# Kernel tuning notes

Hardware: AMD Instinct MI355X
Metric: run time of the kernel (lower is better)

The kernel has to match this reference:

```python
import jax, jax.numpy as jnp
import numpy as np

S = 100   # n_pred_samples
B = 64    # batch
DIMS = [784, 512, 512, 10]


def setup_inputs() -> dict:
    key = jax.random.key(0)
    ks = jax.random.split(key, 16)
    d = {}
    d["inputs"] = jax.random.normal(ks[0], (B, DIMS[0]), dtype=jnp.float32)
    d["task_id"] = 0
    # variational params: means ~ 0.1*N(0,1), logvars constant -6 (as in module init)
    d["wm0"] = jax.random.normal(ks[1], (DIMS[0], DIMS[1])) * 0.1
    d["wv0"] = jnp.full((DIMS[0], DIMS[1]), -6.0, jnp.float32)
    d["bm0"] = jnp.full((DIMS[1],), 0.1, jnp.float32)
    d["bv0"] = jnp.full((DIMS[1],), -6.0, jnp.float32)
    d["wm1"] = jax.random.normal(ks[2], (DIMS[1], DIMS[2])) * 0.1
    d["wv1"] = jnp.full((DIMS[1], DIMS[2]), -6.0, jnp.float32)
    d["bm1"] = jnp.full((DIMS[2],), 0.1, jnp.float32)
    d["bv1"] = jnp.full((DIMS[2],), -6.0, jnp.float32)
    d["wml"] = jax.random.normal(ks[3], (DIMS[2], DIMS[3])) * 0.1
    d["wvl"] = jnp.full((DIMS[2], DIMS[3]), -6.0, jnp.float32)
    d["bml"] = jnp.full((DIMS[3],), 0.1, jnp.float32)
    d["bvl"] = jnp.full((DIMS[3],), -6.0, jnp.float32)
    # reparameterization noise (passed explicitly for determinism)
    d["we0"] = jax.random.normal(ks[4], (S, DIMS[0], DIMS[1]), dtype=jnp.float32)
    d["be0"] = jax.random.normal(ks[5], (S, 1, DIMS[1]), dtype=jnp.float32)
    d["we1"] = jax.random.normal(ks[6], (S, DIMS[1], DIMS[2]), dtype=jnp.float32)
    d["be1"] = jax.random.normal(ks[7], (S, 1, DIMS[2]), dtype=jnp.float32)
    d["wel"] = jax.random.normal(ks[8], (S, DIMS[2], DIMS[3]), dtype=jnp.float32)
    d["bel"] = jax.random.normal(ks[9], (S, 1, DIMS[3]), dtype=jnp.float32)
    return d


def _sample(eps, logvar, mean):
    # reparameterization: eps * exp(0.5*logvar) + mean
    return eps * jnp.exp(0.5 * logvar) + mean


def reference(inputs, task_id, wm0, wv0, bm0, bv0, wm1, wv1, bm1, bv1,
              wml, wvl, bml, bvl, we0, be0, we1, be1, wel, bel):
    # activations: [S, B, D]
    act = jnp.broadcast_to(inputs[None], (S,) + inputs.shape)
    # hidden layer 0
    W0 = _sample(we0, wv0, wm0)          # [S, D0, D1]
    b0 = _sample(be0, bv0, bm0)          # [S, 1, D1]
    act = jax.nn.relu(jnp.einsum('sbi,sio->sbo', act, W0) + b0)
    # hidden layer 1
    W1 = _sample(we1, wv1, wm1)
    b1 = _sample(be1, bv1, bm1)
    act = jax.nn.relu(jnp.einsum('sbi,sio->sbo', act, W1) + b1)
    # last (task-specific) layer: original does broadcast-mul + sum over dim 2,
    # which is exactly a batched matmul — expressed here as an einsum
    Wl = _sample(wel, wvl, wml)          # [S, D2, O]
    bl = _sample(bel, bvl, bml)          # [S, 1, O]
    logits = jnp.einsum('sbh,sho->sbo', act, Wl) + bl   # [S, B, O]
    return logits
```

## Files before the change

### kernel.cpp

```cpp
#include <hip/hip_runtime.h>
#include <hip/hip_bf16.h>


typedef __bf16 bf16x8 __attribute__((ext_vector_type(8)));
typedef float f32x4 __attribute__((ext_vector_type(4)));

#define NSAMP 100
#define BATCH 64
#define D0 784
#define D1 512
#define D2 512
#define DOUT 10
#define K0PAD 800

#define BM 64
#define BN 64
#define BK 32
#define LDK 36

__device__ __forceinline__ unsigned short f2bf(float f) {
    __bf16 b = (__bf16)f;
    return __builtin_bit_cast(unsigned short, b);
}

union FragU { uint2 d[2]; bf16x8 v; };

#define XB_N   (BATCH * K0PAD)
#define SG0_N  (D0 * D1)
#define SG1_N  (D1 * D2)
#define SGL_N  (D2 * DOUT)
#define B0_N   (NSAMP * D1)
#define B1_N   (NSAMP * D2)
#define BL_N   (NSAMP * DOUT)
#define PREP_TOTAL (XB_N + SG0_N + SG1_N + SGL_N + B0_N + B1_N + BL_N)

__global__ __launch_bounds__(256) void prep(
    const float* __restrict__ inputs,
    const float* __restrict__ wv0, const float* __restrict__ wv1,
    const float* __restrict__ wvl,
    const float* __restrict__ be0, const float* __restrict__ bv0, const float* __restrict__ bm0,
    const float* __restrict__ be1, const float* __restrict__ bv1, const float* __restrict__ bm1,
    const float* __restrict__ bel, const float* __restrict__ bvl, const float* __restrict__ bml,
    unsigned short* __restrict__ Xb, float* __restrict__ sigma0,
    float* __restrict__ sigma1, float* __restrict__ sigmal,
    float* __restrict__ bias0, float* __restrict__ bias1, float* __restrict__ biasl)
{
    int i = blockIdx.x * 256 + threadIdx.x;
    if (i < XB_N) {
        int m = i / K0PAD, k = i % K0PAD;
        float v = (k < D0) ? inputs[m * D0 + k] : 0.f;
        Xb[i] = f2bf(v);
        return;
    }
    i -= XB_N;
    if (i < SG0_N) { sigma0[i] = __expf(0.5f * wv0[i]); return; }
    i -= SG0_N;
    if (i < SG1_N) { sigma1[i] = __expf(0.5f * wv1[i]); return; }
    i -= SG1_N;
    if (i < SGL_N) { sigmal[i] = __expf(0.5f * wvl[i]); return; }
    i -= SGL_N;
    if (i < B0_N) { int n = i % D1; bias0[i] = fmaf(be0[i], __expf(0.5f * bv0[n]), bm0[n]); return; }
    i -= B0_N;
    if (i < B1_N) { int n = i % D2; bias1[i] = fmaf(be1[i], __expf(0.5f * bv1[n]), bm1[n]); return; }
    i -= B1_N;
    if (i < BL_N) { int o = i % DOUT; biasl[i] = fmaf(bel[i], __expf(0.5f * bvl[o]), bml[o]); return; }
}

__global__ __launch_bounds__(256) void gemm_layer(
    const unsigned short* __restrict__ A, int lda, long aStride,
    const float* __restrict__ eps, long eStride,
    const float* __restrict__ sigma, const float* __restrict__ mean,
    int N, int K, int Kvalid,
    const float* __restrict__ bias,
    void* __restrict__ outp, int outBf16)
{
    __shared__ unsigned short smA[BM * LDK];
    __shared__ unsigned short smB[BN * LDK];

    const int s  = blockIdx.y;
    const int n0 = blockIdx.x * BN;
    const int t  = threadIdx.x;

    const unsigned short* As = A + (long)s * aStride;
    const float* epsS = eps + (long)s * eStride;

    const int am = t >> 2;
    const int ac = (t & 3) * 8;
    const int bn  = t & 63;
    const int bk0 = (t >> 6) * 8;

    const int lane = t & 63;
    const int w    = t >> 6;
    const int mbase = (w & 1) * 32;
    const int nbase = (w >> 1) * 32;
    const int fr   = lane & 15;
    const int quad = lane >> 4;

    f32x4 acc[2][2] = {};
    const int KT = K / BK;

    uint4 pa;
    float pe[8], ps[8], pm[8];

    {
        pa = *reinterpret_cast<const uint4*>(As + (long)am * lda + ac);
#pragma unroll
        for (int j = 0; j < 8; ++j) {
            int k = bk0 + j;
            long off = (long)k * N + n0 + bn;
            bool v = k < Kvalid;
            pe[j] = v ? epsS[off] : 0.f;
            ps[j] = v ? sigma[off] : 0.f;
            pm[j] = v ? mean[off] : 0.f;
        }
    }

    for (int kt = 0; kt < KT; ++kt) {
        __syncthreads();
        {
            unsigned short* dst = &smA[am * LDK + ac];
            uint2 w0; w0.x = pa.x; w0.y = pa.y;
            uint2 w1; w1.x = pa.z; w1.y = pa.w;
            reinterpret_cast<uint2*>(dst)[0] = w0;
            *reinterpret_cast<uint2*>(dst + 4) = w1;
        }
        {
            unsigned int p01, p23, p45, p67;
            p01 = (unsigned int)f2bf(fmaf(pe[0], ps[0], pm[0])) |
                  ((unsigned int)f2bf(fmaf(pe[1], ps[1], pm[1])) << 16);
            p23 = (unsigned int)f2bf(fmaf(pe[2], ps[2], pm[2])) |
                  ((unsigned int)f2bf(fmaf(pe[3], ps[3], pm[3])) << 16);
            p45 = (unsigned int)f2bf(fmaf(pe[4], ps[4], pm[4])) |
                  ((unsigned int)f2bf(fmaf(pe[5], ps[5], pm[5])) << 16);
            p67 = (unsigned int)f2bf(fmaf(pe[6], ps[6], pm[6])) |
                  ((unsigned int)f2bf(fmaf(pe[7], ps[7], pm[7])) << 16);
            unsigned short* dst = &smB[bn * LDK + bk0];
            uint2 w0; w0.x = p01; w0.y = p23;
            uint2 w1; w1.x = p45; w1.y = p67;
            reinterpret_cast<uint2*>(dst)[0] = w0;
            *reinterpret_cast<uint2*>(dst + 4) = w1;
        }
        if (kt + 1 < KT) {
            const int kg = (kt + 1) * BK;
            pa = *reinterpret_cast<const uint4*>(As + (long)am * lda + kg + ac);
#pragma unroll
            for (int j = 0; j < 8; ++j) {
                int k = kg + bk0 + j;
                long off = (long)k * N + n0 + bn;
                bool v = k < Kvalid;
                pe[j] = v ? epsS[off] : 0.f;
                ps[j] = v ? sigma[off] : 0.f;
                pm[j] = v ? mean[off] : 0.f;
            }
        }
        __syncthreads();
        FragU af[2], bf[2];
#pragma unroll
        for (int mi = 0; mi < 2; ++mi) {
            const unsigned short* p = &smA[(mbase + mi * 16 + fr) * LDK + quad * 8];
            const uint2* q = reinterpret_cast<const uint2*>(p);
            af[mi].d[0] = q[0]; af[mi].d[1] = q[1];
        }
#pragma unroll
        for (int ni = 0; ni < 2; ++ni) {
            const unsigned short* p = &smB[(nbase + ni * 16 + fr) * LDK + quad * 8];
            const uint2* q = reinterpret_cast<const uint2*>(p);
            bf[ni].d[0] = q[0]; bf[ni].d[1] = q[1];
        }
#pragma unroll
        for (int mi = 0; mi < 2; ++mi)
#pragma unroll
            for (int ni = 0; ni < 2; ++ni)
                acc[mi][ni] = __builtin_amdgcn_mfma_f32_16x16x32_bf16(
                    af[mi].v, bf[ni].v, acc[mi][ni], 0, 0, 0);
    }

    const long outBase = (long)s * BATCH * N;
#pragma unroll
    for (int mi = 0; mi < 2; ++mi) {
#pragma unroll
        for (int ni = 0; ni < 2; ++ni) {
            const int col = n0 + nbase + ni * 16 + fr;
            const float bv = bias[(long)s * N + col];
#pragma unroll
            for (int r = 0; r < 4; ++r) {
                const int row = mbase + mi * 16 + quad * 4 + r;
                float v = acc[mi][ni][r] + bv;
                v = fmaxf(v, 0.f);
                const long idx = outBase + (long)row * N + col;
                if (outBf16) ((unsigned short*)outp)[idx] = f2bf(v);
                else         ((float*)outp)[idx] = v;
            }
        }
    }
}

__global__ __launch_bounds__(320) void last_layer(
    const float* __restrict__ act2,
    const float* __restrict__ wel,
    const float* __restrict__ sigmal,
    const float* __restrict__ wml,
    const float* __restrict__ biasl,
    float* __restrict__ out)
{
    __shared__ float smW[D2 * DOUT];
    const int s = blockIdx.x;
    const int t = threadIdx.x;
    const float* we = wel + (long)s * D2 * DOUT;
    for (int i = t; i < D2 * DOUT; i += 320)
        smW[i] = fmaf(we[i], sigmal[i], wml[i]);
    __syncthreads();

    const int m  = t / 5;
    const int op = t % 5;
    const float* a = act2 + ((long)s * BATCH + m) * D2;
    float acc0 = 0.f, acc1 = 0.f;
#pragma unroll 4
    for (int k = 0; k < D2; k += 4) {
        float4 av = *reinterpret_cast<const float4*>(a + k);
        acc0 = fmaf(av.x, smW[(k + 0) * DOUT + op], acc0);
        acc0 = fmaf(av.y, smW[(k + 1) * DOUT + op], acc0);
        acc0 = fmaf(av.z, smW[(k + 2) * DOUT + op], acc0);
        acc0 = fmaf(av.w, smW[(k + 3) * DOUT + op], acc0);
        acc1 = fmaf(av.x, smW[(k + 0) * DOUT + op + 5], acc1);
        acc1 = fmaf(av.y, smW[(k + 1) * DOUT + op + 5], acc1);
        acc1 = fmaf(av.z, smW[(k + 2) * DOUT + op + 5], acc1);
        acc1 = fmaf(av.w, smW[(k + 3) * DOUT + op + 5], acc1);
    }
    const long ob = ((long)s * BATCH + m) * DOUT;
    out[ob + op]     = acc0 + biasl[s * DOUT + op];
    out[ob + op + 5] = acc1 + biasl[s * DOUT + op + 5];
}

extern "C" void kernel_launch(void* const* d_in, const int* in_sizes, int n_in,
                              void* d_out, int out_size, void* d_ws, size_t ws_size,
                              hipStream_t stream)
{
    const float* inputs = (const float*)d_in[0];
    const float* wm0 = (const float*)d_in[2];
    const float* wv0 = (const float*)d_in[3];
    const float* bm0 = (const float*)d_in[4];
    const float* bv0 = (const float*)d_in[5];
    const float* wm1 = (const float*)d_in[6];
    const float* wv1 = (const float*)d_in[7];
    const float* bm1 = (const float*)d_in[8];
    const float* bv1 = (const float*)d_in[9];
    const float* wml = (const float*)d_in[10];
    const float* wvl = (const float*)d_in[11];
    const float* bml = (const float*)d_in[12];
    const float* bvl = (const float*)d_in[13];
    const float* we0 = (const float*)d_in[14];
    const float* be0 = (const float*)d_in[15];
    const float* we1 = (const float*)d_in[16];
    const float* be1 = (const float*)d_in[17];
    const float* wel = (const float*)d_in[18];
    const float* bel = (const float*)d_in[19];

    char* w = (char*)d_ws;
    unsigned short* Xb = (unsigned short*)w; w += (size_t)XB_N * 2;
    float* sigma0 = (float*)w; w += (size_t)SG0_N * 4;
    float* sigma1 = (float*)w; w += (size_t)SG1_N * 4;
    float* sigmal = (float*)w; w += (size_t)SGL_N * 4;
    float* bias0  = (float*)w; w += (size_t)B0_N * 4;
    float* bias1  = (float*)w; w += (size_t)B1_N * 4;
    float* biasl  = (float*)w; w += (size_t)BL_N * 4;
    unsigned short* act1 = (unsigned short*)w; w += (size_t)NSAMP * BATCH * D1 * 2;
    float* act2 = (float*)w; w += (size_t)NSAMP * BATCH * D2 * 4;

    prep<<<dim3((PREP_TOTAL + 255) / 256), 256, 0, stream>>>(
        inputs, wv0, wv1, wvl, be0, bv0, bm0, be1, bv1, bm1, bel, bvl, bml,
        Xb, sigma0, sigma1, sigmal, bias0, bias1, biasl);

    gemm_layer<<<dim3(D1 / BN, NSAMP), 256, 0, stream>>>(
        Xb, K0PAD, 0L, we0, (long)D0 * D1, sigma0, wm0,
        D1, K0PAD, D0, bias0, (void*)act1, 1);

    gemm_layer<<<dim3(D2 / BN, NSAMP), 256, 0, stream>>>(
        act1, D1, (long)BATCH * D1, we1, (long)D1 * D2, sigma1, wm1,
        D2, D1, D1, bias1, (void*)act2, 0);

    last_layer<<<dim3(NSAMP), 320, 0, stream>>>(
        act2, wel, sigmal, wml, biasl, (float*)d_out);
}
```

Measured before the change: 411.0 us.

## Pack sigma/mean as bf16 pairs and use per-wave register GEMM without LDS

Prep now packs the bf16 sigma and bf16 mean for layers 0 and 1 into one 32-bit word, so the GEMM reads one word per weight instead of two floats. The block-tiled LDS GEMM is replaced by a kernel where each wave owns a 16-column strip of one sample across all 64 rows. Fragments load straight from global memory into registers with double-buffered prefetch, and eps uses nontemporal loads, which removes LDS staging and __syncthreads. The cost is that A is reloaded by every wave, and sigma and mean drop to bf16 precision before the reparameterisation FMA.

```diff
diff --git a/kernel.cpp b/kernel.cpp
--- a/kernel.cpp
+++ b/kernel.cpp
@@ -13,36 +13,39 @@
 #define DOUT 10
 #define K0PAD 800
 
-#define BM 64
-#define BN 64
-#define BK 32
-#define LDK 36
-
 __device__ __forceinline__ unsigned short f2bf(float f) {
     __bf16 b = (__bf16)f;
     return __builtin_bit_cast(unsigned short, b);
 }
-
-union FragU { uint2 d[2]; bf16x8 v; };
+__device__ __forceinline__ float bf_hi(unsigned int u) {
+    return __builtin_bit_cast(float, u & 0xffff0000u);
+}
+__device__ __forceinline__ float bf_lo(unsigned int u) {
+    return __builtin_bit_cast(float, u << 16);
+}
+
+union FragU { uint2 d[2]; uint4 q; bf16x8 v; };
 
 #define XB_N   (BATCH * K0PAD)
-#define SG0_N  (D0 * D1)
-#define SG1_N  (D1 * D2)
+#define PS0_N  (D0 * D1)
+#define PS1_N  (D1 * D2)
 #define SGL_N  (D2 * DOUT)
 #define B0_N   (NSAMP * D1)
 #define B1_N   (NSAMP * D2)
 #define BL_N   (NSAMP * DOUT)
-#define PREP_TOTAL (XB_N + SG0_N + SG1_N + SGL_N + B0_N + B1_N + BL_N)
+#define PREP_TOTAL (XB_N + PS0_N + PS1_N + SGL_N + B0_N + B1_N + BL_N)
 
 __global__ __launch_bounds__(256) void prep(
     const float* __restrict__ inputs,
-    const float* __restrict__ wv0, const float* __restrict__ wv1,
+    const float* __restrict__ wv0, const float* __restrict__ wm0,
+    const float* __restrict__ wv1, const float* __restrict__ wm1,
     const float* __restrict__ wvl,
     const float* __restrict__ be0, const float* __restrict__ bv0, const float* __restrict__ bm0,
     const float* __restrict__ be1, const float* __restrict__ bv1, const float* __restrict__ bm1,
     const float* __restrict__ bel, const float* __restrict__ bvl, const float* __restrict__ bml,
-    unsigned short* __restrict__ Xb, float* __restrict__ sigma0,
-    float* __restrict__ sigma1, float* __restrict__ sigmal,
+    unsigned short* __restrict__ Xb,
+    unsigned int* __restrict__ psm0, unsigned int* __restrict__ psm1,
+    float* __restrict__ sigmal,
     float* __restrict__ bias0, float* __restrict__ bias1, float* __restrict__ biasl)
 {
     int i = blockIdx.x * 256 + threadIdx.x;
@@ -53,10 +56,20 @@
         return;
     }
     i -= XB_N;
-    if (i < SG0_N) { sigma0[i] = __expf(0.5f * wv0[i]); return; }
-    i -= SG0_N;
-    if (i < SG1_N) { sigma1[i] = __expf(0.5f * wv1[i]); return; }
-    i -= SG1_N;
+    if (i < PS0_N) {
+        unsigned int sg = f2bf(__expf(0.5f * wv0[i]));
+        unsigned int mn = f2bf(wm0[i]);
+        psm0[i] = (sg << 16) | mn;
+        return;
+    }
+    i -= PS0_N;
+    if (i < PS1_N) {
+        unsigned int sg = f2bf(__expf(0.5f * wv1[i]));
+        unsigned int mn = f2bf(wm1[i]);
+        psm1[i] = (sg << 16) | mn;
+        return;
+    }
+    i -= PS1_N;
     if (i < SGL_N) { sigmal[i] = __expf(0.5f * wvl[i]); return; }
     i -= SGL_N;
     if (i < B0_N) { int n = i % D1; bias0[i] = fmaf(be0[i], __expf(0.5f * bv0[n]), bm0[n]); return; }
@@ -66,131 +79,89 @@
     if (i < BL_N) { int o = i % DOUT; biasl[i] = fmaf(bel[i], __expf(0.5f * bvl[o]), bml[o]); return; }
 }
 
-__global__ __launch_bounds__(256) void gemm_layer(
+__global__ __launch_bounds__(256) void gemm_wave(
     const unsigned short* __restrict__ A, int lda, long aStride,
     const float* __restrict__ eps, long eStride,
-    const float* __restrict__ sigma, const float* __restrict__ mean,
-    int N, int K, int Kvalid,
+    const unsigned int* __restrict__ psm,
+    int KT, int Kvalid,
     const float* __restrict__ bias,
     void* __restrict__ outp, int outBf16)
 {
-    __shared__ unsigned short smA[BM * LDK];
-    __shared__ unsigned short smB[BN * LDK];
-
-    const int s  = blockIdx.y;
-    const int n0 = blockIdx.x * BN;
-    const int t  = threadIdx.x;
-
-    const unsigned short* As = A + (long)s * aStride;
-    const float* epsS = eps + (long)s * eStride;
-
-    const int am = t >> 2;
-    const int ac = (t & 3) * 8;
-    const int bn  = t & 63;
-    const int bk0 = (t >> 6) * 8;
-
-    const int lane = t & 63;
-    const int w    = t >> 6;
-    const int mbase = (w & 1) * 32;
-    const int nbase = (w >> 1) * 32;
+    const int N = 512;
+    const int wid  = blockIdx.x * 4 + (threadIdx.x >> 6);
+    const int s    = wid >> 5;
+    const int n0   = (wid & 31) << 4;
+    const int lane = threadIdx.x & 63;
     const int fr   = lane & 15;
     const int quad = lane >> 4;
 
-    f32x4 acc[2][2] = {};
-    const int KT = K / BK;
-
-    uint4 pa;
-    float pe[8], ps[8], pm[8];
-
-    {
-        pa = *reinterpret_cast<const uint4*>(As + (long)am * lda + ac);
+    const unsigned short* aP = A + (long)s * aStride + (long)fr * lda + quad * 8;
+    const long bbase = (long)(quad * 8) * N + n0 + fr;
+    const float* eP        = eps + (long)s * eStride + bbase;
+    const unsigned int* pP = psm + bbase;
+
+    f32x4 acc[4] = {};
+    const bool tail = (Kvalid < KT * 32);
+
+    uint4 pa0[4], pa1[4];
+    float pe0[8], pe1[8];
+    unsigned int pp0[8], pp1[8];
+
+    auto loadAll = [&](int kt, uint4* pa, float* pe, unsigned int* pp) {
+        const int kb = kt * 32;
+        const bool guard = tail && (kt == KT - 1);
+#pragma unroll
+        for (int sub = 0; sub < 4; ++sub)
+            pa[sub] = *reinterpret_cast<const uint4*>(aP + (long)sub * 16 * lda + kb);
 #pragma unroll
         for (int j = 0; j < 8; ++j) {
-            int k = bk0 + j;
-            long off = (long)k * N + n0 + bn;
-            bool v = k < Kvalid;
-            pe[j] = v ? epsS[off] : 0.f;
-            ps[j] = v ? sigma[off] : 0.f;
-            pm[j] = v ? mean[off] : 0.f;
-        }
-    }
-
-    for (int kt = 0; kt < KT; ++kt) {
-        __syncthreads();
-        {
-            unsigned short* dst = &smA[am * LDK + ac];
-            uint2 w0; w0.x = pa.x; w0.y = pa.y;
-            uint2 w1; w1.x = pa.z; w1.y = pa.w;
-            reinterpret_cast<uint2*>(dst)[0] = w0;
-            *reinterpret_cast<uint2*>(dst + 4) = w1;
-        }
-        {
-            unsigned int p01, p23, p45, p67;
-            p01 = (unsigned int)f2bf(fmaf(pe[0], ps[0], pm[0])) |
-                  ((unsigned int)f2bf(fmaf(pe[1], ps[1], pm[1])) << 16);
-            p23 = (unsigned int)f2bf(fmaf(pe[2], ps[2], pm[2])) |
-                  ((unsigned int)f2bf(fmaf(pe[3], ps[3], pm[3])) << 16);
-            p45 = (unsigned int)f2bf(fmaf(pe[4], ps[4], pm[4])) |
-                  ((unsigned int)f2bf(fmaf(pe[5], ps[5], pm[5])) << 16);
-            p67 = (unsigned int)f2bf(fmaf(pe[6], ps[6], pm[6])) |
-                  ((unsigned int)f2bf(fmaf(pe[7], ps[7], pm[7])) << 16);
-            unsigned short* dst = &smB[bn * LDK + bk0];
-            uint2 w0; w0.x = p01; w0.y = p23;
-            uint2 w1; w1.x = p45; w1.y = p67;
-            reinterpret_cast<uint2*>(dst)[0] = w0;
-            *reinterpret_cast<uint2*>(dst + 4) = w1;
-        }
-        if (kt + 1 < KT) {
-            const int kg = (kt + 1) * BK;
-            pa = *reinterpret_cast<const uint4*>(As + (long)am * lda + kg + ac);
-#pragma unroll
-            for (int j = 0; j < 8; ++j) {
-                int k = kg + bk0 + j;
-                long off = (long)k * N + n0 + bn;
-                bool v = k < Kvalid;
-                pe[j] = v ? epsS[off] : 0.f;
-                ps[j] = v ? sigma[off] : 0.f;
-                pm[j] = v ? mean[off] : 0.f;
-            }
-        }
-        __syncthreads();
-        FragU af[2], bf[2];
-#pragma unroll
-        for (int mi = 0; mi < 2; ++mi) {
-            const unsigned short* p = &smA[(mbase + mi * 16 + fr) * LDK + quad * 8];
-            const uint2* q = reinterpret_cast<const uint2*>(p);
-            af[mi].d[0] = q[0]; af[mi].d[1] = q[1];
-        }
-#pragma unroll
-        for (int ni = 0; ni < 2; ++ni) {
-            const unsigned short* p = &smB[(nbase + ni * 16 + fr) * LDK + quad * 8];
-            const uint2* q = reinterpret_cast<const uint2*>(p);
-            bf[ni].d[0] = q[0]; bf[ni].d[1] = q[1];
-        }
-#pragma unroll
-        for (int mi = 0; mi < 2; ++mi)
-#pragma unroll
-            for (int ni = 0; ni < 2; ++ni)
-                acc[mi][ni] = __builtin_amdgcn_mfma_f32_16x16x32_bf16(
-                    af[mi].v, bf[ni].v, acc[mi][ni], 0, 0, 0);
-    }
-
+            const long off = (long)(kb + j) * N;
+            const bool ok = !guard || (kb + quad * 8 + j) < Kvalid;
+            pe[j] = ok ? __builtin_nontemporal_load(eP + off) : 0.f;
+            pp[j] = ok ? pP[off] : 0u;
+        }
+    };
+
+    auto compute = [&](const uint4* pa, const float* pe, const unsigned int* pp) {
+        unsigned int u[4];
+#pragma unroll
+        for (int h = 0; h < 4; ++h) {
+            float w0 = fmaf(pe[2 * h],     bf_hi(pp[2 * h]),     bf_lo(pp[2 * h]));
+            float w1 = fmaf(pe[2 * h + 1], bf_hi(pp[2 * h + 1]), bf_lo(pp[2 * h + 1]));
+            u[h] = (unsigned int)f2bf(w0) | ((unsigned int)f2bf(w1) << 16);
+        }
+        FragU bf;
+        bf.d[0].x = u[0]; bf.d[0].y = u[1];
+        bf.d[1].x = u[2]; bf.d[1].y = u[3];
+#pragma unroll
+        for (int sub = 0; sub < 4; ++sub) {
+            FragU af; af.q = pa[sub];
+            acc[sub] = __builtin_amdgcn_mfma_f32_16x16x32_bf16(af.v, bf.v, acc[sub], 0, 0, 0);
+        }
+    };
+
+    loadAll(0, pa0, pe0, pp0);
+    int kt = 0;
+    for (; kt + 2 <= KT; kt += 2) {
+        loadAll(kt + 1, pa1, pe1, pp1);
+        compute(pa0, pe0, pp0);
+        if (kt + 2 < KT) loadAll(kt + 2, pa0, pe0, pp0);
+        compute(pa1, pe1, pp1);
+    }
+    if (kt < KT) compute(pa0, pe0, pp0);
+
+    const float bv = bias[(long)s * N + n0 + fr];
     const long outBase = (long)s * BATCH * N;
 #pragma unroll
-    for (int mi = 0; mi < 2; ++mi) {
-#pragma unroll
-        for (int ni = 0; ni < 2; ++ni) {
-            const int col = n0 + nbase + ni * 16 + fr;
-            const float bv = bias[(long)s * N + col];
-#pragma unroll
-            for (int r = 0; r < 4; ++r) {
-                const int row = mbase + mi * 16 + quad * 4 + r;
-                float v = acc[mi][ni][r] + bv;
-                v = fmaxf(v, 0.f);
-                const long idx = outBase + (long)row * N + col;
-                if (outBf16) ((unsigned short*)outp)[idx] = f2bf(v);
-                else         ((float*)outp)[idx] = v;
-            }
+    for (int sub = 0; sub < 4; ++sub) {
+#pragma unroll
+        for (int r = 0; r < 4; ++r) {
+            const int row = sub * 16 + quad * 4 + r;
+            float v = acc[sub][r] + bv;
+            v = fmaxf(v, 0.f);
+            const long idx = outBase + (long)row * N + n0 + fr;
+            if (outBf16) ((unsigned short*)outp)[idx] = f2bf(v);
+            else         ((float*)outp)[idx] = v;
         }
     }
 }
@@ -257,9 +228,9 @@
     const float* bel = (const float*)d_in[19];
 
     char* w = (char*)d_ws;
-    unsigned short* Xb = (unsigned short*)w; w += (size_t)XB_N * 2;
-    float* sigma0 = (float*)w; w += (size_t)SG0_N * 4;
-    float* sigma1 = (float*)w; w += (size_t)SG1_N * 4;
+    unsigned short* Xb  = (unsigned short*)w; w += (size_t)XB_N * 2;
+    unsigned int* psm0  = (unsigned int*)w;   w += (size_t)PS0_N * 4;
+    unsigned int* psm1  = (unsigned int*)w;   w += (size_t)PS1_N * 4;
     float* sigmal = (float*)w; w += (size_t)SGL_N * 4;
     float* bias0  = (float*)w; w += (size_t)B0_N * 4;
     float* bias1  = (float*)w; w += (size_t)B1_N * 4;
@@ -268,16 +239,17 @@
     float* act2 = (float*)w; w += (size_t)NSAMP * BATCH * D2 * 4;
 
     prep<<<dim3((PREP_TOTAL + 255) / 256), 256, 0, stream>>>(
-        inputs, wv0, wv1, wvl, be0, bv0, bm0, be1, bv1, bm1, bel, bvl, bml,
-        Xb, sigma0, sigma1, sigmal, bias0, bias1, biasl);
-
-    gemm_layer<<<dim3(D1 / BN, NSAMP), 256, 0, stream>>>(
-        Xb, K0PAD, 0L, we0, (long)D0 * D1, sigma0, wm0,
-        D1, K0PAD, D0, bias0, (void*)act1, 1);
-
-    gemm_layer<<<dim3(D2 / BN, NSAMP), 256, 0, stream>>>(
-        act1, D1, (long)BATCH * D1, we1, (long)D1 * D2, sigma1, wm1,
-        D2, D1, D1, bias1, (void*)act2, 0);
+        inputs, wv0, wm0, wv1, wm1, wvl,
+        be0, bv0, bm0, be1, bv1, bm1, bel, bvl, bml,
+        Xb, psm0, psm1, sigmal, bias0, bias1, biasl);
+
+    gemm_wave<<<dim3(NSAMP * 32 / 4), 256, 0, stream>>>(
+        Xb, K0PAD, 0L, we0, (long)D0 * D1, psm0,
+        K0PAD / 32, D0, bias0, (void*)act1, 1);
+
+    gemm_wave<<<dim3(NSAMP * 32 / 4), 256, 0, stream>>>(
+        act1, D1, (long)BATCH * D1, we1, (long)D1 * D2, psm1,
+        D1 / 32, D1, bias1, (void*)act2, 0);
 
     last_layer<<<dim3(NSAMP), 320, 0, stream>>>(
         act2, wel, sigmal, wml, biasl, (float*)d_out);
```

Measured after the change: 456.9 us. 11.2% more time.
